# Performance work log

Measured on AMD Instinct MI355X. Metric: run time of the kernel, lower is better.

Reference implementation:

```python
import jax, jax.numpy as jnp
import numpy as np

# Sizes: batch=32, in_channels=32, out_channels=64, grid 256x256, modes1=modes2=32
B, CI, CO, NX, NY, M1, M2 = 32, 32, 64, 256, 256, 32, 32


def setup_inputs() -> dict:
    key = jax.random.key(0)
    k1, k2, k3 = jax.random.split(key, 3)
    scale = 1.0 / (CI * CO)
    return {
        "x": jax.random.normal(k1, (B, CI, NX, NY), dtype=jnp.float32),
        "w_real": scale * jax.random.uniform(k2, (CI, CO, 2 * M1, M2 + 1), dtype=jnp.float32),
        "w_imag": scale * jax.random.uniform(k3, (CI, CO, 2 * M1, M2 + 1), dtype=jnp.float32),
        "modes1": M1,
        "modes2": M2,
    }


def reference(x, w_real, w_imag, modes1, modes2):
    # rfft2 with 'forward' normalization (divide by nx*ny), as in torch.fft.rfft2(norm='forward')
    xf = jnp.fft.rfft2(x, norm="forward")  # (b, i, nx, ny//2+1) complex64
    # resize_rfft2(xf, (2*modes1, 2*modes2)) in the truncation regime (nx >= 2*m1, ny//2+1 >= m2+1):
    # keep first modes2+1 columns (rfft axis) and the first/last modes1 rows (full fft axis).
    xt = jnp.concatenate(
        [xf[..., :modes1, : modes2 + 1], xf[..., -modes1:, : modes2 + 1]], axis=-2
    )  # (b, i, 2*m1, m2+1)
    W = w_real + 1j * w_imag  # (i, o, 2*m1, m2+1) complex
    # complex channel mixing, keep only real part
    y = jnp.einsum("bixy,ioxy->boxy", xt, W).real  # (b, o, 2*m1, m2+1)
    # signed mode-sum: double-count conjugate-symmetric modes, correct the (0,0) DC mode
    out = (
        2.0 * jnp.sum(y[..., :modes1, :], axis=(-2, -1))
        + 2.0 * jnp.sum(y[..., modes1:, 1:], axis=(-2, -1))
        - y[..., 0, 0]
    )  # (b, o)
    return out
```

## Files before the change

### kernel.cpp

```cpp
#include <hip/hip_runtime.h>
#include <hip/hip_bf16.h>
#include <math.h>

#define BATCH 32
#define CIn   32
#define COut  64

typedef __attribute__((ext_vector_type(8))) short bf16x8;
typedef __attribute__((ext_vector_type(4))) float f32x4;

#define OB_T1F  0u
#define OB_ECF  40960u
#define OB_ESF  73728u
#define OB_XTB  106496u
#define OB_PART 8757248u

__device__ __forceinline__ ushort f2bf(float f) {
    union { float f; uint u; } v; v.f = f;
    uint r = (v.u + 0x7FFFu + ((v.u >> 16) & 1u)) >> 16;
    return (ushort)r;
}

__device__ __forceinline__ ushort f2bfn(float f) {
    union { __hip_bfloat16 h; ushort u; } v;
    v.h = __float2bfloat16(f);
    return v.u;
}
__device__ __forceinline__ bf16x8 cvt8(f32x4 lo, f32x4 hi) {
    union { __hip_bfloat162 h2[4]; bf16x8 v; } u;
    u.h2[0] = __float22bfloat162_rn(make_float2(lo[0], lo[1]));
    u.h2[1] = __float22bfloat162_rn(make_float2(lo[2], lo[3]));
    u.h2[2] = __float22bfloat162_rn(make_float2(hi[0], hi[1]));
    u.h2[3] = __float22bfloat162_rn(make_float2(hi[2], hi[3]));
    return u.v;
}

#define NB0 0
#define NB1 16
#define NB2 32
#define NB3 48
#define NB4 50

__global__ void fno_tw(ushort* __restrict__ T1f, ushort* __restrict__ Ecf,
                       ushort* __restrict__ Esf) {
    const int nb[5] = {NB0, NB1, NB2, NB3, NB4};
    int idx = blockIdx.x * 256 + threadIdx.x;
    const float w0 = 6.28318530717958647692f / 256.0f;
    if (idx < 20480) {
        int i = idx & 7, l = (idx >> 3) & 63, ct = idx >> 9;
        int c = ct / 5, t = ct - 5 * c;
        int k = 32 * c + 8 * (l >> 4) + i;
        int n = nb[t] + (l & 15);
        int ky = n >> 1, s = n & 1;
        int m = (k * ky) & 255;
        float v = s ? -sinf(w0 * (float)m) : cosf(w0 * (float)m);
        T1f[idx] = f2bf(v * (1.0f / 65536.0f));
    }
    if (idx < 16384) {
        int i = idx & 7, l = (idx >> 3) & 63, km = idx >> 9;
        int ks = km >> 2, mt = km & 3;
        int xx = ks * 32 + ((l >> 4) << 3) + i;
        int kx = mt * 16 + (l & 15);
        int kxa = (kx < 32) ? kx : kx + 192;
        int m = (xx * kxa) & 255;
        Ecf[idx] = f2bf(cosf(w0 * (float)m));
        Esf[idx] = f2bf(-sinf(w0 * (float)m));
    }
}

#define MFMA5(KC, AV)                                                              \
    acc0 = __builtin_amdgcn_mfma_f32_16x16x32_bf16((AV), bfr[(KC)*5+0], acc0, 0,0,0); \
    acc1 = __builtin_amdgcn_mfma_f32_16x16x32_bf16((AV), bfr[(KC)*5+1], acc1, 0,0,0); \
    acc2 = __builtin_amdgcn_mfma_f32_16x16x32_bf16((AV), bfr[(KC)*5+2], acc2, 0,0,0); \
    acc3 = __builtin_amdgcn_mfma_f32_16x16x32_bf16((AV), bfr[(KC)*5+3], acc3, 0,0,0); \
    acc4 = __builtin_amdgcn_mfma_f32_16x16x32_bf16((AV), bfr[(KC)*5+4], acc4, 0,0,0);

#define STAGE_CG(CG) do {                                                          \
    int cg_ = (CG);                                                                \
    int sl_ = cg_ >> 3, kc_ = cg_ & 7;                                             \
    _Pragma("unroll")                                                              \
    for (int j = 0; j < 2; ++j) {                                                  \
        int rws_ = 8 * j + (lane >> 3);                                            \
        int sg_  = (lane & 7) ^ (rws_ & 7);                                        \
        const float* gp_ = x + ((size_t)p * 256 + sl_ * 64 + w * 16 + rws_) * 256  \
                             + kc_ * 32 + (sg_ << 2);                              \
        char* lp_ = (char*)&smx[cg_ & 3][0] + w * 2048 + j * 1024 + (lane << 4);   \
        __builtin_amdgcn_global_load_lds(                                          \
            (const __attribute__((address_space(1))) unsigned int*)gp_,            \
            (__attribute__((address_space(3))) unsigned int*)lp_, 16, 0, 0);       \
    } } while (0)

#define DSR(CG, RA, RB) do {                                                       \
    const char* base_ = (const char*)&smx[(CG) & 3][0] + w * 2048 + r0 * 128;      \
    (RA) = *(const f32x4*)(base_ + ((((g << 1)    ) ^ xr) << 4));                  \
    (RB) = *(const f32x4*)(base_ + ((((g << 1) + 1) ^ xr) << 4));                  \
    } while (0)

#define WAITV(N) do {                                                              \
    asm volatile("s_waitcnt vmcnt(" #N ")" ::: "memory");                          \
    __builtin_amdgcn_sched_barrier(0); } while (0)

#define WAITL0 do {                                                                \
    asm volatile("s_waitcnt lgkmcnt(0)" ::: "memory");                             \
    __builtin_amdgcn_sched_barrier(0); } while (0)

#define YTW(ACC, T) do {                                                           \
    int n_ = nb[T] + r0;                                                           \
    if ((T) != 4 || r0 >= 14) {                                                    \
        _Pragma("unroll")                                                          \
        for (int j = 0; j < 4; ++j) {                                              \
            int xrow_ = sl * 64 + w * 16 + 4 * g + j;                              \
            int us_ = n_ * 256 + ((((xrow_ >> 3) ^ (n_ & 31)) << 3) | (xrow_ & 7));\
            Yt[us_] = f2bfn((ACC)[j]);                                             \
        } } } while (0)

__global__ __launch_bounds__(256, 2)
void fno_fused(const float* __restrict__ x, const ushort* __restrict__ T1f,
               const ushort* __restrict__ Ecf, const ushort* __restrict__ Esf,
               ushort* __restrict__ XTb) {
    __shared__ float smx[4][2048];
    __shared__ __align__(16) ushort Yt[16896];
    const int nb[5] = {NB0, NB1, NB2, NB3, NB4};
    const int tid  = threadIdx.x;
    const int lane = tid & 63;
    const int w    = tid >> 6;
    const int r0   = lane & 15;
    const int g    = lane >> 4;
    const int xr   = r0 & 7;
    const int p    = blockIdx.x;

    bf16x8 bfr[40];
    const bf16x8* bp = (const bf16x8*)T1f;
#pragma unroll
    for (int q = 0; q < 40; ++q) bfr[q] = bp[q * 64 + lane];

    f32x4 rA[2][2];

    STAGE_CG(0); STAGE_CG(1); STAGE_CG(2);
    WAITV(4);
    DSR(0, rA[0][0], rA[0][1]);

    f32x4 acc0, acc1, acc2, acc3, acc4;
#pragma unroll
    for (int cg = 0; cg < 32; ++cg) {
        if ((cg & 7) == 0) {
            acc0 = (f32x4){0,0,0,0}; acc1 = (f32x4){0,0,0,0};
            acc2 = (f32x4){0,0,0,0}; acc3 = (f32x4){0,0,0,0};
            acc4 = (f32x4){0,0,0,0};
        }
        WAITL0;
        bf16x8 af = cvt8(rA[cg & 1][0], rA[cg & 1][1]);
        if (cg + 3 < 32) STAGE_CG(cg + 3);
        if (cg <= 28)      { WAITV(4); }
        else if (cg == 29) { WAITV(2); }
        else if (cg == 30) { WAITV(0); }
        if (cg + 1 < 32) DSR(cg + 1, rA[(cg + 1) & 1][0], rA[(cg + 1) & 1][1]);
        MFMA5(cg & 7, af);
        if ((cg & 7) == 7) {
            int sl = cg >> 3;
            YTW(acc0, 0); YTW(acc1, 1); YTW(acc2, 2); YTW(acc3, 3); YTW(acc4, 4);
        }
    }
    __syncthreads();

    const int mt = w;
    f32x4 P1[5], P2[5];
#pragma unroll
    for (int t = 0; t < 5; ++t) { P1[t] = (f32x4){0,0,0,0}; P2[t] = (f32x4){0,0,0,0}; }

    const bf16x8* ecp = (const bf16x8*)Ecf;
    const bf16x8* esp = (const bf16x8*)Esf;
#pragma unroll
    for (int ks = 0; ks < 8; ++ks) {
        bf16x8 ea = ecp[(ks * 4 + mt) * 64 + lane];
        bf16x8 es = esp[(ks * 4 + mt) * 64 + lane];
#pragma unroll
        for (int t = 0; t < 5; ++t) {
            int n = nb[t] + r0;
            bf16x8 b = *(const bf16x8*)&Yt[n * 256 + ((((ks << 2) + g) ^ (n & 31)) << 3)];
            P1[t] = __builtin_amdgcn_mfma_f32_16x16x32_bf16(ea, b, P1[t], 0, 0, 0);
            P2[t] = __builtin_amdgcn_mfma_f32_16x16x32_bf16(es, b, P2[t], 0, 0, 0);
        }
    }

    ushort* xtl = (ushort*)&smx[0][0];
#pragma unroll
    for (int t = 0; t < 5; ++t) {
        int n  = nb[t] + r0;
        int ky = n >> 1, im = n & 1;
#pragma unroll
        for (int j = 0; j < 4; ++j) {
            float v2x = __shfl_xor(P2[t][j], 1);
            if (t == 4 && r0 < 14) continue;
            int kx = mt * 16 + 4 * g + j;
            float val = im ? (P1[t][j] + v2x) : (P1[t][j] - v2x);
            float wgt = (kx < 32) ? ((kx == 0 && ky == 0) ? 1.f : 2.f)
                                  : ((ky == 0) ? 0.f : 2.f);
            if (im) wgt = -wgt;
            xtl[kx * 66 + n] = f2bfn(wgt * val);
        }
    }
    __syncthreads();

    const uint4* srcq = (const uint4*)xtl;
    uint4* dstq = (uint4*)(XTb + (size_t)p * 4224);
    for (int e = tid; e < 528; e += 256) dstq[e] = srcq[e];
}

__global__ __launch_bounds__(256)
void fno_gemm3(const ushort* __restrict__ XTb, const float* __restrict__ Wr,
               const float* __restrict__ Wi, float* __restrict__ part) {
    const int blk = blockIdx.x;
    const int ic  = blk / 22;
    const int sc  = blk - ic * 22;
    const int tid = threadIdx.x;
    const int lane = tid & 63;
    const int w    = tid >> 6;
    const int r0   = lane & 15;
    const int g    = lane >> 4;
    const int o    = (w << 4) + r0;

    const float* wrp = Wr + ((size_t)ic * 64 + o) * 2112 + sc * 96 + 4 * g;
    const float* wip = Wi + ((size_t)ic * 64 + o) * 2112 + sc * 96 + 4 * g;
    const ushort* a0 = XTb + ((size_t)r0 * 32 + ic) * 4224 + sc * 192 + 8 * g;
    const ushort* a1 = a0 + (size_t)16 * 32 * 4224;

    f32x4 acc0 = {0,0,0,0}, acc1 = {0,0,0,0};
#pragma unroll
    for (int st = 0; st < 6; ++st) {
        f32x4 vr = *(const f32x4*)(wrp + st * 16);
        f32x4 vi = *(const f32x4*)(wip + st * 16);
        union { __hip_bfloat162 h2[4]; bf16x8 v; } ub;
        ub.h2[0] = __float22bfloat162_rn(make_float2(vr[0], vi[0]));
        ub.h2[1] = __float22bfloat162_rn(make_float2(vr[1], vi[1]));
        ub.h2[2] = __float22bfloat162_rn(make_float2(vr[2], vi[2]));
        ub.h2[3] = __float22bfloat162_rn(make_float2(vr[3], vi[3]));
        bf16x8 af0 = *(const bf16x8*)(a0 + st * 32);
        bf16x8 af1 = *(const bf16x8*)(a1 + st * 32);
        acc0 = __builtin_amdgcn_mfma_f32_16x16x32_bf16(af0, ub.v, acc0, 0, 0, 0);
        acc1 = __builtin_amdgcn_mfma_f32_16x16x32_bf16(af1, ub.v, acc1, 0, 0, 0);
    }

    float* pp = part + (size_t)blk * 2048;
#pragma unroll
    for (int j = 0; j < 4; ++j) {
        pp[(4 * g + j) * 64 + o]      = acc0[j];
        pp[(16 + 4 * g + j) * 64 + o] = acc1[j];
    }
}

__global__ __launch_bounds__(256)
void fno_reduce(const float* __restrict__ part, float* __restrict__ out) {
    __shared__ float red[256];
    const int tid = threadIdx.x;
    const int il  = tid & 7;
    const int js  = tid >> 3;
    const int idx = blockIdx.x * 8 + il;

    float s = 0.f;
#pragma unroll
    for (int t = 0; t < 22; ++t)
        s += part[(size_t)(js + 32 * t) * 2048 + idx];
    red[tid] = s;
    __syncthreads();

    if (tid < 8) {
        float v = 0.f;
#pragma unroll
        for (int q = 0; q < 32; ++q) v += red[q * 8 + tid];
        out[blockIdx.x * 8 + tid] = v;
    }
}

extern "C" void kernel_launch(void* const* d_in, const int* in_sizes, int n_in,
                              void* d_out, int out_size, void* d_ws, size_t ws_size,
                              hipStream_t stream) {
    const float* x  = (const float*)d_in[0];
    const float* wr = (const float*)d_in[1];
    const float* wi = (const float*)d_in[2];
    float* out = (float*)d_out;
    char* ws   = (char*)d_ws;

    ushort* T1f = (ushort*)(ws + OB_T1F);
    ushort* Ecf = (ushort*)(ws + OB_ECF);
    ushort* Esf = (ushort*)(ws + OB_ESF);
    ushort* XTb = (ushort*)(ws + OB_XTB);
    float* part = (float*)(ws + OB_PART);

    fno_tw<<<80, 256, 0, stream>>>(T1f, Ecf, Esf);
    fno_fused<<<1024, 256, 0, stream>>>(x, T1f, Ecf, Esf, XTb);
    fno_gemm3<<<704, 256, 0, stream>>>(XTb, wr, wi, part);
    fno_reduce<<<256, 256, 0, stream>>>(part, out);
}
```

Before: 80.30 us.

## Stage 64-column x chunks with double buffer and pack Yt bf16 stores

```diff
diff --git a/kernel.cpp b/kernel.cpp
--- a/kernel.cpp
+++ b/kernel.cpp
@@ -75,25 +75,29 @@
     acc3 = __builtin_amdgcn_mfma_f32_16x16x32_bf16((AV), bfr[(KC)*5+3], acc3, 0,0,0); \
     acc4 = __builtin_amdgcn_mfma_f32_16x16x32_bf16((AV), bfr[(KC)*5+4], acc4, 0,0,0);
 
-#define STAGE_CG(CG) do {                                                          \
-    int cg_ = (CG);                                                                \
-    int sl_ = cg_ >> 3, kc_ = cg_ & 7;                                             \
+#define STAGE_SC(SC) do {                                                          \
+    int sc_ = (SC);                                                                \
+    const float* gb_ = x + ((size_t)p * 256 + (sc_ >> 2) * 64 + w * 16) * 256      \
+                         + (sc_ & 3) * 64;                                         \
+    char* lb_ = (char*)&smx[sc_ & 1][0] + w * 4096;                                \
     _Pragma("unroll")                                                              \
-    for (int j = 0; j < 2; ++j) {                                                  \
-        int rws_ = 8 * j + (lane >> 3);                                            \
-        int sg_  = (lane & 7) ^ (rws_ & 7);                                        \
-        const float* gp_ = x + ((size_t)p * 256 + sl_ * 64 + w * 16 + rws_) * 256  \
-                             + kc_ * 32 + (sg_ << 2);                              \
-        char* lp_ = (char*)&smx[cg_ & 3][0] + w * 2048 + j * 1024 + (lane << 4);   \
+    for (int j = 0; j < 4; ++j) {                                                  \
+        int row_ = 4 * j + (lane >> 4);                                            \
+        int sg_  = (lane & 15) ^ (row_ & 7);                                       \
+        const float* gp_ = gb_ + (size_t)row_ * 256 + (sg_ << 2);                  \
+        char* lp_ = lb_ + j * 1024;                                                \
         __builtin_amdgcn_global_load_lds(                                          \
             (const __attribute__((address_space(1))) unsigned int*)gp_,            \
             (__attribute__((address_space(3))) unsigned int*)lp_, 16, 0, 0);       \
     } } while (0)
 
-#define DSR(CG, RA, RB) do {                                                       \
-    const char* base_ = (const char*)&smx[(CG) & 3][0] + w * 2048 + r0 * 128;      \
-    (RA) = *(const f32x4*)(base_ + ((((g << 1)    ) ^ xr) << 4));                  \
-    (RB) = *(const f32x4*)(base_ + ((((g << 1) + 1) ^ xr) << 4));                  \
+#define DSR4(SC) do {                                                              \
+    const char* db_ = (const char*)&smx[(SC) & 1][0] + w * 4096 + r0 * 256;        \
+    f32x4* rp_ = rr[(SC) & 1];                                                     \
+    rp_[0] = *(const f32x4*)(db_ + (((((g << 1)    )) ^ xr) << 4));                \
+    rp_[1] = *(const f32x4*)(db_ + (((((g << 1) + 1)) ^ xr) << 4));                \
+    rp_[2] = *(const f32x4*)(db_ + ((8 + (((g << 1)    ) ^ xr)) << 4));            \
+    rp_[3] = *(const f32x4*)(db_ + ((8 + (((g << 1) + 1) ^ xr)) << 4));            \
     } while (0)
 
 #define WAITV(N) do {                                                              \
@@ -104,21 +108,22 @@
     asm volatile("s_waitcnt lgkmcnt(0)" ::: "memory");                             \
     __builtin_amdgcn_sched_barrier(0); } while (0)
 
-#define YTW(ACC, T) do {                                                           \
+#define YTWP(ACC, T) do {                                                          \
     int n_ = nb[T] + r0;                                                           \
     if ((T) != 4 || r0 >= 14) {                                                    \
-        _Pragma("unroll")                                                          \
-        for (int j = 0; j < 4; ++j) {                                              \
-            int xrow_ = sl * 64 + w * 16 + 4 * g + j;                              \
-            int us_ = n_ * 256 + ((((xrow_ >> 3) ^ (n_ & 31)) << 3) | (xrow_ & 7));\
-            Yt[us_] = f2bfn((ACC)[j]);                                             \
-        } } } while (0)
+        int xr0_ = sl * 64 + w * 16 + 4 * g;                                       \
+        int us_ = n_ * 256 + ((((xr0_ >> 3) ^ (n_ & 31)) << 3) | (xr0_ & 7));      \
+        union { __hip_bfloat162 h[2]; uint2 u; } uu_;                              \
+        uu_.h[0] = __float22bfloat162_rn(make_float2((ACC)[0], (ACC)[1]));         \
+        uu_.h[1] = __float22bfloat162_rn(make_float2((ACC)[2], (ACC)[3]));         \
+        *(uint2*)&Yt[us_] = uu_.u;                                                 \
+    } } while (0)
 
 __global__ __launch_bounds__(256, 2)
 void fno_fused(const float* __restrict__ x, const ushort* __restrict__ T1f,
                const ushort* __restrict__ Ecf, const ushort* __restrict__ Esf,
                ushort* __restrict__ XTb) {
-    __shared__ float smx[4][2048];
+    __shared__ float smx[2][4096];
     __shared__ __align__(16) ushort Yt[16896];
     const int nb[5] = {NB0, NB1, NB2, NB3, NB4};
     const int tid  = threadIdx.x;
@@ -134,31 +139,34 @@
 #pragma unroll
     for (int q = 0; q < 40; ++q) bfr[q] = bp[q * 64 + lane];
 
-    f32x4 rA[2][2];
-
-    STAGE_CG(0); STAGE_CG(1); STAGE_CG(2);
+    f32x4 rr[2][4];
+
+    STAGE_SC(0); STAGE_SC(1);
     WAITV(4);
-    DSR(0, rA[0][0], rA[0][1]);
+    DSR4(0);
 
     f32x4 acc0, acc1, acc2, acc3, acc4;
 #pragma unroll
-    for (int cg = 0; cg < 32; ++cg) {
-        if ((cg & 7) == 0) {
+    for (int it = 0; it < 16; ++it) {
+        if ((it & 3) == 0) {
             acc0 = (f32x4){0,0,0,0}; acc1 = (f32x4){0,0,0,0};
             acc2 = (f32x4){0,0,0,0}; acc3 = (f32x4){0,0,0,0};
             acc4 = (f32x4){0,0,0,0};
         }
         WAITL0;
-        bf16x8 af = cvt8(rA[cg & 1][0], rA[cg & 1][1]);
-        if (cg + 3 < 32) STAGE_CG(cg + 3);
-        if (cg <= 28)      { WAITV(4); }
-        else if (cg == 29) { WAITV(2); }
-        else if (cg == 30) { WAITV(0); }
-        if (cg + 1 < 32) DSR(cg + 1, rA[(cg + 1) & 1][0], rA[(cg + 1) & 1][1]);
-        MFMA5(cg & 7, af);
-        if ((cg & 7) == 7) {
-            int sl = cg >> 3;
-            YTW(acc0, 0); YTW(acc1, 1); YTW(acc2, 2); YTW(acc3, 3); YTW(acc4, 4);
+        if (it + 2 < 16) STAGE_SC(it + 2);
+        if (it <= 13)      { WAITV(4); }
+        else if (it == 14) { WAITV(0); }
+        if (it < 15) DSR4(it + 1);
+
+        bf16x8 a0v = cvt8(rr[it & 1][0], rr[it & 1][1]);
+        bf16x8 a1v = cvt8(rr[it & 1][2], rr[it & 1][3]);
+        MFMA5(2 * (it & 3)    , a0v);
+        MFMA5(2 * (it & 3) + 1, a1v);
+
+        if ((it & 3) == 3) {
+            int sl = it >> 2;
+            YTWP(acc0, 0); YTWP(acc1, 1); YTWP(acc2, 2); YTWP(acc3, 3); YTWP(acc4, 4);
         }
     }
     __syncthreads();
```

Result: no change. 79.20 us, median of 2 (-1.4%).

## Restructure first-stage DFT so each wave owns an output tile over shared row slabs

Applied to the files above, without the earlier changes.

```diff
diff --git a/kernel.cpp b/kernel.cpp
--- a/kernel.cpp
+++ b/kernel.cpp
@@ -21,11 +21,6 @@
     return (ushort)r;
 }
 
-__device__ __forceinline__ ushort f2bfn(float f) {
-    union { __hip_bfloat16 h; ushort u; } v;
-    v.h = __float2bfloat16(f);
-    return v.u;
-}
 __device__ __forceinline__ bf16x8 cvt8(f32x4 lo, f32x4 hi) {
     union { __hip_bfloat162 h2[4]; bf16x8 v; } u;
     u.h2[0] = __float22bfloat162_rn(make_float2(lo[0], lo[1]));
@@ -33,6 +28,11 @@
     u.h2[2] = __float22bfloat162_rn(make_float2(hi[0], hi[1]));
     u.h2[3] = __float22bfloat162_rn(make_float2(hi[2], hi[3]));
     return u.v;
+}
+__device__ __forceinline__ ushort f2bfn(float f) {
+    union { __hip_bfloat16 h; ushort u; } v;
+    v.h = __float2bfloat16(f);
+    return v.u;
 }
 
 #define NB0 0
@@ -68,57 +68,34 @@
     }
 }
 
-#define MFMA5(KC, AV)                                                              \
-    acc0 = __builtin_amdgcn_mfma_f32_16x16x32_bf16((AV), bfr[(KC)*5+0], acc0, 0,0,0); \
-    acc1 = __builtin_amdgcn_mfma_f32_16x16x32_bf16((AV), bfr[(KC)*5+1], acc1, 0,0,0); \
-    acc2 = __builtin_amdgcn_mfma_f32_16x16x32_bf16((AV), bfr[(KC)*5+2], acc2, 0,0,0); \
-    acc3 = __builtin_amdgcn_mfma_f32_16x16x32_bf16((AV), bfr[(KC)*5+3], acc3, 0,0,0); \
-    acc4 = __builtin_amdgcn_mfma_f32_16x16x32_bf16((AV), bfr[(KC)*5+4], acc4, 0,0,0);
-
-#define STAGE_CG(CG) do {                                                          \
-    int cg_ = (CG);                                                                \
-    int sl_ = cg_ >> 3, kc_ = cg_ & 7;                                             \
+#define STAGE_S(S) do {                                                            \
+    int s_ = (S);                                                                  \
+    float* lb_ = &smx[s_ & 1][0];                                                  \
+    const float* gb_ = x + ((size_t)p * 256 + s_ * 16) * 256;                      \
     _Pragma("unroll")                                                              \
-    for (int j = 0; j < 2; ++j) {                                                  \
-        int rws_ = 8 * j + (lane >> 3);                                            \
-        int sg_  = (lane & 7) ^ (rws_ & 7);                                        \
-        const float* gp_ = x + ((size_t)p * 256 + sl_ * 64 + w * 16 + rws_) * 256  \
-                             + kc_ * 32 + (sg_ << 2);                              \
-        char* lp_ = (char*)&smx[cg_ & 3][0] + w * 2048 + j * 1024 + (lane << 4);   \
+    for (int jj = 0; jj < 4; ++jj) {                                               \
+        int rl_ = w * 4 + jj;                                                      \
+        int sg_ = lane ^ (rl_ & 7);             \
+        const float* gp_ = gb_ + (size_t)rl_ * 256 + (sg_ << 2);                   \
+        char* lp_ = (char*)lb_ + (rl_ << 10);                                      \
         __builtin_amdgcn_global_load_lds(                                          \
             (const __attribute__((address_space(1))) unsigned int*)gp_,            \
             (__attribute__((address_space(3))) unsigned int*)lp_, 16, 0, 0);       \
     } } while (0)
 
-#define DSR(CG, RA, RB) do {                                                       \
-    const char* base_ = (const char*)&smx[(CG) & 3][0] + w * 2048 + r0 * 128;      \
-    (RA) = *(const f32x4*)(base_ + ((((g << 1)    ) ^ xr) << 4));                  \
-    (RB) = *(const f32x4*)(base_ + ((((g << 1) + 1) ^ xr) << 4));                  \
-    } while (0)
-
 #define WAITV(N) do {                                                              \
     asm volatile("s_waitcnt vmcnt(" #N ")" ::: "memory");                          \
     __builtin_amdgcn_sched_barrier(0); } while (0)
 
-#define WAITL0 do {                                                                \
-    asm volatile("s_waitcnt lgkmcnt(0)" ::: "memory");                             \
+#define BAR do {                                                                   \
+    __builtin_amdgcn_s_barrier();                                                  \
     __builtin_amdgcn_sched_barrier(0); } while (0)
-
-#define YTW(ACC, T) do {                                                           \
-    int n_ = nb[T] + r0;                                                           \
-    if ((T) != 4 || r0 >= 14) {                                                    \
-        _Pragma("unroll")                                                          \
-        for (int j = 0; j < 4; ++j) {                                              \
-            int xrow_ = sl * 64 + w * 16 + 4 * g + j;                              \
-            int us_ = n_ * 256 + ((((xrow_ >> 3) ^ (n_ & 31)) << 3) | (xrow_ & 7));\
-            Yt[us_] = f2bfn((ACC)[j]);                                             \
-        } } } while (0)
 
 __global__ __launch_bounds__(256, 2)
 void fno_fused(const float* __restrict__ x, const ushort* __restrict__ T1f,
                const ushort* __restrict__ Ecf, const ushort* __restrict__ Esf,
                ushort* __restrict__ XTb) {
-    __shared__ float smx[4][2048];
+    __shared__ __align__(16) float smx[2][4096];
     __shared__ __align__(16) ushort Yt[16896];
     const int nb[5] = {NB0, NB1, NB2, NB3, NB4};
     const int tid  = threadIdx.x;
@@ -129,37 +106,56 @@
     const int xr   = r0 & 7;
     const int p    = blockIdx.x;
 
-    bf16x8 bfr[40];
+    bf16x8 bfr0[8], bfr4[8];
     const bf16x8* bp = (const bf16x8*)T1f;
 #pragma unroll
-    for (int q = 0; q < 40; ++q) bfr[q] = bp[q * 64 + lane];
-
-    f32x4 rA[2][2];
-
-    STAGE_CG(0); STAGE_CG(1); STAGE_CG(2);
+    for (int c = 0; c < 8; ++c) bfr0[c] = bp[(c * 5 + w) * 64 + lane];
+    if (w == 3) {
+#pragma unroll
+        for (int c = 0; c < 8; ++c) bfr4[c] = bp[(c * 5 + 4) * 64 + lane];
+    }
+
+    STAGE_S(0); STAGE_S(1);
     WAITV(4);
-    DSR(0, rA[0][0], rA[0][1]);
-
-    f32x4 acc0, acc1, acc2, acc3, acc4;
-#pragma unroll
-    for (int cg = 0; cg < 32; ++cg) {
-        if ((cg & 7) == 0) {
-            acc0 = (f32x4){0,0,0,0}; acc1 = (f32x4){0,0,0,0};
-            acc2 = (f32x4){0,0,0,0}; acc3 = (f32x4){0,0,0,0};
-            acc4 = (f32x4){0,0,0,0};
-        }
-        WAITL0;
-        bf16x8 af = cvt8(rA[cg & 1][0], rA[cg & 1][1]);
-        if (cg + 3 < 32) STAGE_CG(cg + 3);
-        if (cg <= 28)      { WAITV(4); }
-        else if (cg == 29) { WAITV(2); }
-        else if (cg == 30) { WAITV(0); }
-        if (cg + 1 < 32) DSR(cg + 1, rA[(cg + 1) & 1][0], rA[(cg + 1) & 1][1]);
-        MFMA5(cg & 7, af);
-        if ((cg & 7) == 7) {
-            int sl = cg >> 3;
-            YTW(acc0, 0); YTW(acc1, 1); YTW(acc2, 2); YTW(acc3, 3); YTW(acc4, 4);
-        }
+    BAR;
+
+    for (int s = 0; s < 16; ++s) {
+        f32x4 a0 = {0, 0, 0, 0}, a4 = {0, 0, 0, 0};
+        const char* rowb = (const char*)&smx[s & 1][0] + (r0 << 10);
+#pragma unroll
+        for (int c = 0; c < 8; ++c) {
+            f32x4 lo = *(const f32x4*)(rowb + ((((c << 3) + (g << 1)    ) ^ xr) << 4));
+            f32x4 hi = *(const f32x4*)(rowb + ((((c << 3) + (g << 1) + 1) ^ xr) << 4));
+            bf16x8 a = cvt8(lo, hi);
+            a0 = __builtin_amdgcn_mfma_f32_16x16x32_bf16(a, bfr0[c], a0, 0, 0, 0);
+            if (w == 3)
+                a4 = __builtin_amdgcn_mfma_f32_16x16x32_bf16(a, bfr4[c], a4, 0, 0, 0);
+        }
+        {
+            int xr0 = (s << 4) + (g << 2);
+            int n0  = nb[w] + r0;
+            int us0 = n0 * 256 + ((((xr0 >> 3) ^ (n0 & 31)) << 3) | (xr0 & 7));
+            union { __hip_bfloat162 h[2]; uint2 u; } uu;
+            uu.h[0] = __float22bfloat162_rn(make_float2(a0[0], a0[1]));
+            uu.h[1] = __float22bfloat162_rn(make_float2(a0[2], a0[3]));
+            *(uint2*)&Yt[us0] = uu.u;
+            if (w == 3 && r0 >= 14) {
+                int n4  = 50 + r0;
+                int us4 = n4 * 256 + ((((xr0 >> 3) ^ (n4 & 31)) << 3) | (xr0 & 7));
+                union { __hip_bfloat162 h[2]; uint2 u; } vv;
+                vv.h[0] = __float22bfloat162_rn(make_float2(a4[0], a4[1]));
+                vv.h[1] = __float22bfloat162_rn(make_float2(a4[2], a4[3]));
+                *(uint2*)&Yt[us4] = vv.u;
+            }
+        }
+        BAR;
+        if (s + 2 < 16) {
+            STAGE_S(s + 2);
+            WAITV(4);
+        } else {
+            WAITV(0);
+        }
+        BAR;
     }
     __syncthreads();
 
```

New measurement: 80.55 us. No clear change (+0.3%).
